# Optimization experiments

Hardware: AMD Instinct MI355X
Metric: run time of the kernel (lower is better)

The kernel has to match this reference:

```python
import jax, jax.numpy as jnp
import numpy as np
import math

B, H, S, DK = 4, 16, 2048, 64

def setup_inputs() -> dict:
    key = jax.random.key(0)
    kq, kk, kv, km = jax.random.split(key, 4)
    Q = jax.random.normal(kq, (B, H, S, DK), dtype=jnp.float32)
    K = jax.random.normal(kk, (B, H, S, DK), dtype=jnp.float32)
    V = jax.random.normal(kv, (B, H, S, DK), dtype=jnp.float32)
    # boolean mask [B, Sq, Sk]; True positions are masked out (set to -1e9)
    mask = jax.random.randint(km, (B, S, S), 0, 2).astype(jnp.bool_)
    return {"Q": Q, "K": K, "V": V, "mask": mask}

def reference(Q, K, V, mask):
    d_k = Q.shape[-1]
    # [B,H,Sq,Sk] scores
    scores = jnp.einsum('bhqd,bhkd->bhqk', Q, K) / math.sqrt(d_k)
    # mask [B,Sq,Sk] broadcasts over head dim (torch code repeats over heads)
    scores = jnp.where(mask[:, None, :, :], jnp.float32(-1e9), scores)
    attn = jax.nn.softmax(scores, axis=-1)
    out = jnp.einsum('bhqk,bhkd->bhqd', attn, V)
    return (out, attn)
```

## Files before the change

kernel.cpp:

```cpp
#include <hip/hip_runtime.h>
#include <cstdint>
#include <cstddef>

#define S_LEN 2048
#define DKD   64
#define BQ    64
#define BK    128
#define NKT   16
#define BDIM  256

typedef float f32x4 __attribute__((ext_vector_type(4)));
typedef short s16x8 __attribute__((ext_vector_type(8)));
typedef short s16x4 __attribute__((ext_vector_type(4)));
typedef unsigned int u32x4 __attribute__((ext_vector_type(4)));
typedef unsigned short u16t;
typedef unsigned long long u64t;

#define KS_OFF    0
#define KT_BYTES  (BK * DKD * 2)
#define VT_OFF    16384
#define VT_BYTES  (DKD * BK * 2)
#define PS_OFF    32768
#define PS_STRIDE 280
#define SMEM_SZ   (PS_OFF + BQ * PS_STRIDE)

__device__ __forceinline__ u16t f2bf(float f) {
  unsigned u = __builtin_bit_cast(unsigned, f);
  return (u16t)((u + 0x7FFFu + ((u >> 16) & 1u)) >> 16);
}
__device__ __forceinline__ float bf_lo(unsigned u) {
  return __builtin_bit_cast(float, u << 16);
}
__device__ __forceinline__ float bf_hi(unsigned u) {
  return __builtin_bit_cast(float, u & 0xFFFF0000u);
}

__device__ __forceinline__ void gl_lds16(const void* g, void* l) {
  typedef __attribute__((address_space(1))) void gvoid;
  typedef __attribute__((address_space(3))) void lvoid;
  __builtin_amdgcn_global_load_lds((gvoid*)(void*)g, (lvoid*)l, 16, 0, 0);
}

#define BAR_VM(N) do { asm volatile("s_waitcnt vmcnt(" #N ")\n\ts_barrier" ::: "memory"); \
                       __builtin_amdgcn_sched_barrier(0); } while (0)
#define BAR_LG()  do { asm volatile("s_waitcnt lgkmcnt(0)\n\ts_barrier" ::: "memory"); \
                       __builtin_amdgcn_sched_barrier(0); } while (0)
#define BAR_VM8() do { asm volatile("s_waitcnt vmcnt(8) lgkmcnt(0)\n\ts_barrier" ::: "memory"); \
                       __builtin_amdgcn_sched_barrier(0); } while (0)

__global__ __launch_bounds__(256)
void prologue(const unsigned char* __restrict__ Mg, const float* __restrict__ Kg,
              const float* __restrict__ Vg, u64t* __restrict__ bits,
              u16t* __restrict__ Kws, u16t* __restrict__ Vws) {
  __shared__ float scr[BK][DKD + 1];
  __shared__ int mflag_s;
  const int tid = threadIdx.x;
  const int bid = blockIdx.x;

  if (bid < 1024) {
    int f = 0;
    for (int i = tid; i < 4096; i += 256) if ((i & 3) && Mg[i]) f = 1;
    if (tid == 0) mflag_s = 0;
    __syncthreads();
    if (f) mflag_s = 1;
    __syncthreads();
    const int mstride = mflag_s ? 1 : 4;

    const int row = bid * 8 + (tid >> 5);
    const int wd  = tid & 31;
    const size_t kbase = (size_t)row * S_LEN + (size_t)wd * 64;
    u64t word = 0;
    if (mstride == 1) {
      const u64t* p = (const u64t*)(Mg + kbase);
      #pragma unroll
      for (int i = 0; i < 8; ++i) {
        u64t x = p[i];
        u64t nz = x | (x >> 4); nz |= nz >> 2; nz |= nz >> 1;
        nz &= 0x0101010101010101ull;
        word |= ((nz * 0x0102040810204080ull) >> 56) << (8 * i);
      }
    } else {
      const unsigned* p = (const unsigned*)Mg + kbase;
      #pragma unroll
      for (int i = 0; i < 64; ++i) word |= (u64t)(p[i] ? 1u : 0u) << i;
    }
    bits[(size_t)row * 32 + wd] = word;
  } else if (bid < 2048) {
    const int kb = bid - 1024;
    const float* src = Kg + (size_t)kb * (BK * DKD);
    u16t* dst = Kws + (size_t)kb * (BK * DKD);
    #pragma unroll
    for (int i = 0; i < 4; ++i) {
      int c = tid + 256 * i;
      int row = c >> 3, y = c & 7;
      int oc = y ^ (row & 7);
      const float4* s4 = (const float4*)(src + row * DKD + 8 * oc);
      float4 a = s4[0], b = s4[1];
      s16x8 h = { (short)f2bf(a.x), (short)f2bf(a.y), (short)f2bf(a.z), (short)f2bf(a.w),
                  (short)f2bf(b.x), (short)f2bf(b.y), (short)f2bf(b.z), (short)f2bf(b.w) };
      *(s16x8*)(dst + row * DKD + 8 * y) = h;
    }
  } else {
    const int vb = bid - 2048;
    const float4* src = (const float4*)(Vg + (size_t)vb * (BK * DKD));
    #pragma unroll
    for (int i = 0; i < 8; ++i) {
      int c = tid + 256 * i;
      float4 v = src[c];
      int k = c >> 4, d0 = (c & 15) * 4;
      scr[k][d0] = v.x; scr[k][d0 + 1] = v.y; scr[k][d0 + 2] = v.z; scr[k][d0 + 3] = v.w;
    }
    __syncthreads();
    u16t* dst = Vws + (size_t)vb * (DKD * BK);
    #pragma unroll
    for (int i = 0; i < 8; ++i) {
      int c = tid + 256 * i;
      int dv = c >> 5, y = c & 31;
      int k0 = 4 * (y ^ (dv & 7));
      ushort4 h = make_ushort4(f2bf(scr[k0][dv]), f2bf(scr[k0 + 1][dv]),
                               f2bf(scr[k0 + 2][dv]), f2bf(scr[k0 + 3][dv]));
      *(ushort4*)(dst + dv * BK + 4 * y) = h;
    }
  }
}

__global__ __launch_bounds__(256)
void attn_ws(const float* __restrict__ Qg, const u16t* __restrict__ Kws,
             const u16t* __restrict__ Vws, const u64t* __restrict__ bits,
             float* __restrict__ outg, float* __restrict__ attng) {
  __shared__ char smem[SMEM_SZ];
  const int tid = threadIdx.x;
  const int p = blockIdx.x;
  const int qb = (p >> 3) & 31;
  const int bh = (p & 7) + 8 * (p >> 8);
  const int b  = bh >> 4;
  const int lane = tid & 63, wv = tid >> 6;
  const int cl = lane & 15, g = lane >> 4;
  const int qrow = qb * BQ + 16 * wv + cl;
  const int swzK = (cl & 7) << 4;
  const int swzV = (cl & 7) << 3;

  const char* Kbh = (const char*)Kws + (size_t)bh * NKT * KT_BYTES;
  const char* Vbh = (const char*)Vws + (size_t)bh * NKT * VT_BYTES;
  const u64t* bitR = bits + (size_t)(b * S_LEN + qrow) * 32;
  float* attnQ = attng + ((size_t)bh * S_LEN + (size_t)qb * BQ) * S_LEN;

  float* oRow[4];
  #pragma unroll
  for (int r = 0; r < 4; ++r)
    oRow[r] = outg + (size_t)(bh * S_LEN + qb * BQ + 16 * wv + 4 * g + r) * DKD + cl;

  s16x8 aq0, aq1;
  {
    const float* qr = Qg + ((size_t)bh * S_LEN + qrow) * DKD;
    float x[8], y[8];
    *(float4*)(x)     = *(const float4*)(qr + 8 * g);
    *(float4*)(x + 4) = *(const float4*)(qr + 8 * g + 4);
    *(float4*)(y)     = *(const float4*)(qr + 32 + 8 * g);
    *(float4*)(y + 4) = *(const float4*)(qr + 32 + 8 * g + 4);
    #pragma unroll
    for (int j = 0; j < 8; ++j) { aq0[j] = (short)f2bf(x[j]); aq1[j] = (short)f2bf(y[j]); }
  }

  auto stageK = [&](int kt, int off) {
    const char* src = Kbh + (size_t)kt * KT_BYTES + wv * 4096 + lane * 16;
    #pragma unroll
    for (int t = 0; t < 4; ++t)
      gl_lds16(src + t * 1024, (void*)(smem + off + wv * 4096 + t * 1024));
  };
  auto stageV = [&](int kt) {
    const char* src = Vbh + (size_t)kt * VT_BYTES + wv * 4096 + lane * 16;
    #pragma unroll
    for (int t = 0; t < 4; ++t)
      gl_lds16(src + t * 1024, (void*)(smem + VT_OFF + wv * 4096 + t * 1024));
  };

  float lsum = 0.f;
  stageK(0, KS_OFF);
  for (int kt = 0; kt < NKT; ++kt) {
    const int cur = (kt & 1) ? VT_OFF : KS_OFF;
    if (kt + 1 < NKT) {
      stageK(kt + 1, (kt & 1) ? KS_OFF : VT_OFF);
      BAR_VM(4);
    } else {
      BAR_VM(0);
    }
    ulonglong2 bw = *(const ulonglong2*)(bitR + 2 * kt);
    #pragma unroll
    for (int s = 0; s < 8; ++s) {
      const char* rb = smem + cur + (16 * s + cl) * 128;
      s16x8 k0 = *(const s16x8*)(rb + ((16 * g) ^ swzK));
      s16x8 k1 = *(const s16x8*)(rb + ((64 + 16 * g) ^ swzK));
      f32x4 acc = {0.f, 0.f, 0.f, 0.f};
      acc = __builtin_amdgcn_mfma_f32_16x16x32_bf16(k0, aq0, acc, 0, 0, 0);
      acc = __builtin_amdgcn_mfma_f32_16x16x32_bf16(k1, aq1, acc, 0, 0, 0);
      unsigned nib = (unsigned)(((s < 4) ? bw.x : bw.y) >> (16 * (s & 3) + 4 * g)) & 0xFu;
      #pragma unroll
      for (int r = 0; r < 4; ++r)
        lsum += ((nib >> r) & 1) ? 0.f : __expf(acc[r] * 0.125f);
    }
    BAR_LG();
  }
  lsum += __shfl_xor(lsum, 16);
  lsum += __shfl_xor(lsum, 32);
  const float rinv = 1.f / lsum;

  f32x4 accpv[4];
  #pragma unroll
  for (int db = 0; db < 4; ++db) accpv[db] = (f32x4){0.f, 0.f, 0.f, 0.f};

  stageK(0, KS_OFF);
  stageV(0);
  BAR_VM(0);
  for (int kt = 0; kt < NKT; ++kt) {
    ulonglong2 bw = *(const ulonglong2*)(bitR + 2 * kt);
    char* pbase = smem + PS_OFF + (16 * wv + cl) * PS_STRIDE;

    #pragma unroll
    for (int ks = 0; ks < 4; ++ks) {
      f32x4 qa[2];
      #pragma unroll
      for (int sp = 0; sp < 2; ++sp) {
        int s = 2 * ks + sp;
        const char* rb = smem + KS_OFF + (16 * s + cl) * 128;
        s16x8 k0 = *(const s16x8*)(rb + ((16 * g) ^ swzK));
        s16x8 k1 = *(const s16x8*)(rb + ((64 + 16 * g) ^ swzK));
        f32x4 acc = {0.f, 0.f, 0.f, 0.f};
        acc = __builtin_amdgcn_mfma_f32_16x16x32_bf16(k0, aq0, acc, 0, 0, 0);
        acc = __builtin_amdgcn_mfma_f32_16x16x32_bf16(k1, aq1, acc, 0, 0, 0);
        qa[sp] = acc;
      }
      unsigned hw[4];
      #pragma unroll
      for (int sp = 0; sp < 2; ++sp) {
        int s = 2 * ks + sp;
        unsigned nib = (unsigned)(((s < 4) ? bw.x : bw.y) >> (16 * (s & 3) + 4 * g)) & 0xFu;
        #pragma unroll
        for (int rr = 0; rr < 2; ++rr) {
          float p0 = ((nib >> (2 * rr)) & 1)     ? 0.f : __expf(qa[sp][2 * rr] * 0.125f) * rinv;
          float p1 = ((nib >> (2 * rr + 1)) & 1) ? 0.f : __expf(qa[sp][2 * rr + 1] * 0.125f) * rinv;
          hw[2 * sp + rr] = (unsigned)f2bf(p0) | ((unsigned)f2bf(p1) << 16);
        }
      }
      *(uint2*)(pbase + 64 * ks + 8 * g)      = make_uint2(hw[0], hw[1]);
      *(uint2*)(pbase + 64 * ks + 32 + 8 * g) = make_uint2(hw[2], hw[3]);
      s16x8 pa = __builtin_bit_cast(s16x8, (u32x4){hw[0], hw[1], hw[2], hw[3]});
      #pragma unroll
      for (int db = 0; db < 4; ++db) {
        const char* vrow = smem + VT_OFF + (16 * db + cl) * 256;
        s16x4 v0 = *(const s16x4*)(vrow + ((64 * ks + 8 * g) ^ swzV));
        s16x4 v1 = *(const s16x4*)(vrow + ((64 * ks + 32 + 8 * g) ^ swzV));
        s16x8 vb = __builtin_shufflevector(v0, v1, 0, 1, 2, 3, 4, 5, 6, 7);
        accpv[db] = __builtin_amdgcn_mfma_f32_16x16x32_bf16(pa, vb, accpv[db], 0, 0, 0);
      }
    }

    BAR_LG();

    if (kt + 1 < NKT) { stageK(kt + 1, KS_OFF); stageV(kt + 1); }

    #pragma unroll
    for (int i = 0; i < 4; ++i) {
      int c = tid + 256 * i;
      int q = c >> 4, ch = c & 15;
      u32x4 d = *(const u32x4*)(smem + PS_OFF + q * PS_STRIDE + ch * 16);
      f32x4 lo = { bf_lo(d.x), bf_hi(d.x), bf_lo(d.y), bf_hi(d.y) };
      f32x4 hi = { bf_lo(d.z), bf_hi(d.z), bf_lo(d.w), bf_hi(d.w) };
      float* dst = attnQ + (size_t)q * S_LEN + kt * BK + ch * 8;
      __builtin_nontemporal_store(lo, (f32x4*)dst);
      __builtin_nontemporal_store(hi, (f32x4*)(dst + 4));
    }

    if (kt + 1 < NKT) BAR_VM8();
  }

  #pragma unroll
  for (int db = 0; db < 4; ++db)
    #pragma unroll
    for (int r = 0; r < 4; ++r)
      oRow[r][16 * db] = accpv[db][r];
}

#define FB_KSTR 144
#define FB_VOFF (BK * FB_KSTR)
#define FB_VSTR 272
#define FB_POFF (FB_VOFF + DKD * FB_VSTR)
#define FB_SMEM (FB_POFF + BQ * FB_VSTR)

__global__ __launch_bounds__(256)
void attn_fb(const float* __restrict__ Qg, const float* __restrict__ Kg,
             const float* __restrict__ Vg, const unsigned char* __restrict__ Mg,
             float* __restrict__ outg, float* __restrict__ attng) {
  __shared__ char smem[FB_SMEM];
  __shared__ int mflag_s;
  const int tid = threadIdx.x;
  const int p = blockIdx.x;
  const int qb = (p >> 3) & 31;
  const int bh = (p & 7) + 8 * (p >> 8);
  const int b  = bh >> 4;

  int f = 0;
  for (int i = tid; i < 4096; i += BDIM) if ((i & 3) && Mg[i]) f = 1;
  if (tid == 0) mflag_s = 0;
  __syncthreads();
  if (f) mflag_s = 1;
  __syncthreads();
  const int mstride = mflag_s ? 1 : 4;

  const int lane = tid & 63, wv = tid >> 6;
  const int cl = lane & 15, g = lane >> 4;
  const int q0 = qb * BQ + 16 * wv + 4 * g;

  const float* Kbh = Kg + (size_t)bh * S_LEN * DKD;
  const float* Vbh = Vg + (size_t)bh * S_LEN * DKD;

  float* aRow[4]; float* oRow[4]; const unsigned char* mRow[4];
  #pragma unroll
  for (int r = 0; r < 4; ++r) {
    aRow[r] = attng + (size_t)(bh * S_LEN + q0 + r) * S_LEN + cl;
    oRow[r] = outg + (size_t)(bh * S_LEN + q0 + r) * DKD + cl;
    mRow[r] = Mg + ((size_t)(b * S_LEN + q0 + r) * S_LEN + cl) * (size_t)mstride;
  }

  s16x8 aq0, aq1;
  {
    const float* qrow = Qg + ((size_t)bh * S_LEN + qb * BQ + 16 * wv + cl) * DKD;
    float x[8], y[8];
    *(float4*)(x)     = *(const float4*)(qrow + 8 * g);
    *(float4*)(x + 4) = *(const float4*)(qrow + 8 * g + 4);
    *(float4*)(y)     = *(const float4*)(qrow + 32 + 8 * g);
    *(float4*)(y + 4) = *(const float4*)(qrow + 32 + 8 * g + 4);
    #pragma unroll
    for (int j = 0; j < 8; ++j) { aq0[j] = (short)f2bf(x[j]); aq1[j] = (short)f2bf(y[j]); }
  }

  float lsum[4] = {0.f, 0.f, 0.f, 0.f};
  for (int kt = 0; kt < NKT; ++kt) {
    const float4* ksrc = (const float4*)(Kbh + (size_t)kt * (BK * DKD));
    #pragma unroll
    for (int it = 0; it < 8; ++it) {
      int c = tid + BDIM * it;
      float4 v = ksrc[c];
      *(ushort4*)(smem + (c >> 4) * FB_KSTR + (c & 15) * 8) =
          make_ushort4(f2bf(v.x), f2bf(v.y), f2bf(v.z), f2bf(v.w));
    }
    __syncthreads();
    #pragma unroll
    for (int s = 0; s < 8; ++s) {
      s16x8 b0 = *(const s16x8*)(smem + (16 * s + cl) * FB_KSTR + 16 * g);
      s16x8 b1 = *(const s16x8*)(smem + (16 * s + cl) * FB_KSTR + 64 + 16 * g);
      f32x4 acc = {0.f, 0.f, 0.f, 0.f};
      acc = __builtin_amdgcn_mfma_f32_16x16x32_bf16(aq0, b0, acc, 0, 0, 0);
      acc = __builtin_amdgcn_mfma_f32_16x16x32_bf16(aq1, b1, acc, 0, 0, 0);
      #pragma unroll
      for (int r = 0; r < 4; ++r) {
        bool mk = mRow[r][(size_t)(kt * BK + 16 * s) * mstride] != 0;
        lsum[r] += mk ? 0.f : __expf(acc[r] * 0.125f);
      }
    }
    __syncthreads();
  }
  float rinv[4];
  #pragma unroll
  for (int r = 0; r < 4; ++r) {
    float l = lsum[r];
    #pragma unroll
    for (int d = 1; d < 16; d <<= 1) l += __shfl_xor(l, d);
    rinv[r] = 1.f / l;
  }

  f32x4 accpv[4];
  #pragma unroll
  for (int db = 0; db < 4; ++db) accpv[db] = (f32x4){0.f, 0.f, 0.f, 0.f};

  for (int kt = 0; kt < NKT; ++kt) {
    const float4* ksrc = (const float4*)(Kbh + (size_t)kt * (BK * DKD));
    #pragma unroll
    for (int it = 0; it < 8; ++it) {
      int c = tid + BDIM * it;
      float4 v = ksrc[c];
      *(ushort4*)(smem + (c >> 4) * FB_KSTR + (c & 15) * 8) =
          make_ushort4(f2bf(v.x), f2bf(v.y), f2bf(v.z), f2bf(v.w));
    }
    const float4* vsrc = (const float4*)(Vbh + (size_t)kt * (BK * DKD));
    #pragma unroll
    for (int it = 0; it < 8; ++it) {
      int c = tid + BDIM * it;
      float4 v = vsrc[c];
      int k = c >> 4, d0 = (c & 15) * 4;
      *(u16t*)(smem + FB_VOFF + (d0 + 0) * FB_VSTR + k * 2) = f2bf(v.x);
      *(u16t*)(smem + FB_VOFF + (d0 + 1) * FB_VSTR + k * 2) = f2bf(v.y);
      *(u16t*)(smem + FB_VOFF + (d0 + 2) * FB_VSTR + k * 2) = f2bf(v.z);
      *(u16t*)(smem + FB_VOFF + (d0 + 3) * FB_VSTR + k * 2) = f2bf(v.w);
    }
    __syncthreads();

    #pragma unroll
    for (int ks = 0; ks < 4; ++ks) {
      f32x4 qa[2];
      #pragma unroll
      for (int sp = 0; sp < 2; ++sp) {
        int s = 2 * ks + sp;
        s16x8 b0 = *(const s16x8*)(smem + (16 * s + cl) * FB_KSTR + 16 * g);
        s16x8 b1 = *(const s16x8*)(smem + (16 * s + cl) * FB_KSTR + 64 + 16 * g);
        f32x4 acc = {0.f, 0.f, 0.f, 0.f};
        acc = __builtin_amdgcn_mfma_f32_16x16x32_bf16(aq0, b0, acc, 0, 0, 0);
        acc = __builtin_amdgcn_mfma_f32_16x16x32_bf16(aq1, b1, acc, 0, 0, 0);
        qa[sp] = acc;
      }
      #pragma unroll
      for (int sp = 0; sp < 2; ++sp) {
        int s = 2 * ks + sp;
        #pragma unroll
        for (int r = 0; r < 4; ++r) {
          bool mk = mRow[r][(size_t)(kt * BK + 16 * s) * mstride] != 0;
          float pv = mk ? 0.f : __expf(qa[sp][r] * 0.125f) * rinv[r];
          __builtin_nontemporal_store(pv, aRow[r] + kt * BK + 16 * s);
          *(u16t*)(smem + FB_POFF + (16 * wv + 4 * g + r) * FB_VSTR +
                   (32 * ks + 16 * sp + cl) * 2) = f2bf(pv);
        }
      }
      s16x4 p0 = *(const s16x4*)(smem + FB_POFF + (16 * wv + cl) * FB_VSTR + (32 * ks + 4 * g) * 2);
      s16x4 p1 = *(const s16x4*)(smem + FB_POFF + (16 * wv + cl) * FB_VSTR + (32 * ks + 16 + 4 * g) * 2);
      s16x8 pa = __builtin_shufflevector(p0, p1, 0, 1, 2, 3, 4, 5, 6, 7);
      #pragma unroll
      for (int db = 0; db < 4; ++db) {
        s16x4 v0 = *(const s16x4*)(smem + FB_VOFF + (16 * db + cl) * FB_VSTR + (32 * ks + 4 * g) * 2);
        s16x4 v1 = *(const s16x4*)(smem + FB_VOFF + (16 * db + cl) * FB_VSTR + (32 * ks + 16 + 4 * g) * 2);
        s16x8 vb = __builtin_shufflevector(v0, v1, 0, 1, 2, 3, 4, 5, 6, 7);
        accpv[db] = __builtin_amdgcn_mfma_f32_16x16x32_bf16(pa, vb, accpv[db], 0, 0, 0);
      }
    }
    __syncthreads();
  }

  #pragma unroll
  for (int db = 0; db < 4; ++db)
    #pragma unroll
    for (int r = 0; r < 4; ++r)
      oRow[r][16 * db] = accpv[db][r];
}

extern "C" void kernel_launch(void* const* d_in, const int* in_sizes, int n_in,
                              void* d_out, int out_size, void* d_ws, size_t ws_size,
                              hipStream_t stream) {
  const float* Q = (const float*)d_in[0];
  const float* K = (const float*)d_in[1];
  const float* V = (const float*)d_in[2];
  const unsigned char* M = (const unsigned char*)d_in[3];
  float* out = (float*)d_out;
  float* attn = out + (size_t)4 * 16 * S_LEN * DKD;

  const size_t BITS_SZ = (size_t)4 * S_LEN * 32 * 8;
  const size_t KWS_SZ  = (size_t)64 * NKT * BK * DKD * 2;
  const size_t VWS_SZ  = (size_t)64 * NKT * DKD * BK * 2;
  if (ws_size >= BITS_SZ + KWS_SZ + VWS_SZ) {
    u64t* bits = (u64t*)d_ws;
    u16t* Kws = (u16t*)((char*)d_ws + BITS_SZ);
    u16t* Vws = (u16t*)((char*)d_ws + BITS_SZ + KWS_SZ);
    prologue<<<3072, 256, 0, stream>>>(M, K, V, bits, Kws, Vws);
    attn_ws<<<2048, BDIM, 0, stream>>>(Q, Kws, Vws, bits, out, attn);
  } else {
    attn_fb<<<2048, BDIM, 0, stream>>>(Q, K, V, M, out, attn);
  }
}
```

Before: 348.5 us.

## Process four query strips per block, fusing next strip's row-sum pass into current PV pass

Each block now handles four consecutive 64-row query strips instead of one, and the grid shrinks to 512 blocks. The row-sum (first) pass for strip st is folded into the second pass of strip st-1, so K tiles are loaded from LDS once and used for both, removing a separate K sweep per strip. The goal is to cut redundant K staging and barriers. In exchange it adds extra MFMA and exp work inside the main loop and leaves fewer blocks to fill the GPU's CUs.

After: 362.8 us. 4.1% more time.

```diff
diff --git a/kernel.cpp b/kernel.cpp
--- a/kernel.cpp
+++ b/kernel.cpp
@@ -8,6 +8,7 @@
 #define BK    128
 #define NKT   16
 #define BDIM  256
+#define NSTRIP 4
 
 typedef float f32x4 __attribute__((ext_vector_type(4)));
 typedef short s16x8 __attribute__((ext_vector_type(8)));
@@ -47,6 +48,21 @@
                        __builtin_amdgcn_sched_barrier(0); } while (0)
 #define BAR_VM8() do { asm volatile("s_waitcnt vmcnt(8) lgkmcnt(0)\n\ts_barrier" ::: "memory"); \
                        __builtin_amdgcn_sched_barrier(0); } while (0)
+
+__device__ __forceinline__ void stage_k(const char* Kbh, int kt, char* smem, int off,
+                                        int wv, int lane) {
+  const char* src = Kbh + (size_t)kt * KT_BYTES + wv * 4096 + lane * 16;
+  #pragma unroll
+  for (int t = 0; t < 4; ++t)
+    gl_lds16(src + t * 1024, (void*)(smem + off + wv * 4096 + t * 1024));
+}
+__device__ __forceinline__ void stage_v(const char* Vbh, int kt, char* smem,
+                                        int wv, int lane) {
+  const char* src = Vbh + (size_t)kt * VT_BYTES + wv * 4096 + lane * 16;
+  #pragma unroll
+  for (int t = 0; t < 4; ++t)
+    gl_lds16(src + t * 1024, (void*)(smem + VT_OFF + wv * 4096 + t * 1024));
+}
 
 __global__ __launch_bounds__(256)
 void prologue(const unsigned char* __restrict__ Mg, const float* __restrict__ Kg,
@@ -124,6 +140,92 @@
   }
 }
 
+template <bool PH1>
+__device__ __forceinline__ void run_round(
+    char* smem, const char* Kbh, const char* Vbh,
+    const u64t* bitA, const u64t* bitB,
+    s16x8 aqA0, s16x8 aqA1, s16x8 aqB0, s16x8 aqB1,
+    float rinvA, float& lsumB, f32x4 (&accpv)[4],
+    float* attnA, int tid, int wv, int lane, int cl, int g, int swzK, int swzV)
+{
+  for (int kt = 0; kt < NKT; ++kt) {
+    ulonglong2 bwA = *(const ulonglong2*)(bitA + 2 * kt);
+    ulonglong2 bwB;
+    if (PH1) bwB = *(const ulonglong2*)(bitB + 2 * kt);
+    char* pbase = smem + PS_OFF + (16 * wv + cl) * PS_STRIDE;
+
+    #pragma unroll
+    for (int ks = 0; ks < 4; ++ks) {
+      f32x4 qa[2];
+      #pragma unroll
+      for (int sp = 0; sp < 2; ++sp) {
+        int s = 2 * ks + sp;
+        const char* rb = smem + KS_OFF + (16 * s + cl) * 128;
+        s16x8 k0 = *(const s16x8*)(rb + ((16 * g) ^ swzK));
+        s16x8 k1 = *(const s16x8*)(rb + ((64 + 16 * g) ^ swzK));
+        f32x4 a = {0.f, 0.f, 0.f, 0.f};
+        a = __builtin_amdgcn_mfma_f32_16x16x32_bf16(k0, aqA0, a, 0, 0, 0);
+        a = __builtin_amdgcn_mfma_f32_16x16x32_bf16(k1, aqA1, a, 0, 0, 0);
+        qa[sp] = a;
+        if (PH1) {
+          f32x4 bb = {0.f, 0.f, 0.f, 0.f};
+          bb = __builtin_amdgcn_mfma_f32_16x16x32_bf16(k0, aqB0, bb, 0, 0, 0);
+          bb = __builtin_amdgcn_mfma_f32_16x16x32_bf16(k1, aqB1, bb, 0, 0, 0);
+          unsigned nib = (unsigned)(((s < 4) ? bwB.x : bwB.y) >> (16 * (s & 3) + 4 * g)) & 0xFu;
+          #pragma unroll
+          for (int r = 0; r < 4; ++r)
+            lsumB += ((nib >> r) & 1) ? 0.f : __expf(bb[r] * 0.125f);
+        }
+      }
+      unsigned hw[4];
+      #pragma unroll
+      for (int sp = 0; sp < 2; ++sp) {
+        int s = 2 * ks + sp;
+        unsigned nib = (unsigned)(((s < 4) ? bwA.x : bwA.y) >> (16 * (s & 3) + 4 * g)) & 0xFu;
+        #pragma unroll
+        for (int rr = 0; rr < 2; ++rr) {
+          float p0 = ((nib >> (2 * rr)) & 1)     ? 0.f : __expf(qa[sp][2 * rr] * 0.125f) * rinvA;
+          float p1 = ((nib >> (2 * rr + 1)) & 1) ? 0.f : __expf(qa[sp][2 * rr + 1] * 0.125f) * rinvA;
+          hw[2 * sp + rr] = (unsigned)f2bf(p0) | ((unsigned)f2bf(p1) << 16);
+        }
+      }
+      *(uint2*)(pbase + 64 * ks + 8 * g)      = make_uint2(hw[0], hw[1]);
+      *(uint2*)(pbase + 64 * ks + 32 + 8 * g) = make_uint2(hw[2], hw[3]);
+      s16x8 pa = __builtin_bit_cast(s16x8, (u32x4){hw[0], hw[1], hw[2], hw[3]});
+      #pragma unroll
+      for (int db = 0; db < 4; ++db) {
+        const char* vrow = smem + VT_OFF + (16 * db + cl) * 256;
+        s16x4 v0 = *(const s16x4*)(vrow + ((64 * ks + 8 * g) ^ swzV));
+        s16x4 v1 = *(const s16x4*)(vrow + ((64 * ks + 32 + 8 * g) ^ swzV));
+        s16x8 vb = __builtin_shufflevector(v0, v1, 0, 1, 2, 3, 4, 5, 6, 7);
+        accpv[db] = __builtin_amdgcn_mfma_f32_16x16x32_bf16(pa, vb, accpv[db], 0, 0, 0);
+      }
+    }
+
+    BAR_LG();
+
+    if (PH1 || kt + 1 < NKT) {
+      int nk = (kt + 1) & (NKT - 1);
+      stage_k(Kbh, nk, smem, KS_OFF, wv, lane);
+      stage_v(Vbh, nk, smem, wv, lane);
+    }
+
+    #pragma unroll
+    for (int i = 0; i < 4; ++i) {
+      int c = tid + 256 * i;
+      int q = c >> 4, ch = c & 15;
+      u32x4 d = *(const u32x4*)(smem + PS_OFF + q * PS_STRIDE + ch * 16);
+      f32x4 lo = { bf_lo(d.x), bf_hi(d.x), bf_lo(d.y), bf_hi(d.y) };
+      f32x4 hi = { bf_lo(d.z), bf_hi(d.z), bf_lo(d.w), bf_hi(d.w) };
+      float* dst = attnA + (size_t)q * S_LEN + kt * BK + ch * 8;
+      __builtin_nontemporal_store(lo, (f32x4*)dst);
+      __builtin_nontemporal_store(hi, (f32x4*)(dst + 4));
+    }
+
+    BAR_VM8();
+  }
+}
+
 __global__ __launch_bounds__(256)
 void attn_ws(const float* __restrict__ Qg, const u16t* __restrict__ Kws,
              const u16t* __restrict__ Vws, const u64t* __restrict__ bits,
@@ -131,27 +233,19 @@
   __shared__ char smem[SMEM_SZ];
   const int tid = threadIdx.x;
   const int p = blockIdx.x;
-  const int qb = (p >> 3) & 31;
-  const int bh = (p & 7) + 8 * (p >> 8);
-  const int b  = bh >> 4;
+  const int sub = (p >> 3) & 7;
+  const int bh  = (p & 7) + 8 * (p >> 6);
+  const int b   = bh >> 4;
   const int lane = tid & 63, wv = tid >> 6;
   const int cl = lane & 15, g = lane >> 4;
-  const int qrow = qb * BQ + 16 * wv + cl;
   const int swzK = (cl & 7) << 4;
   const int swzV = (cl & 7) << 3;
 
   const char* Kbh = (const char*)Kws + (size_t)bh * NKT * KT_BYTES;
   const char* Vbh = (const char*)Vws + (size_t)bh * NKT * VT_BYTES;
-  const u64t* bitR = bits + (size_t)(b * S_LEN + qrow) * 32;
-  float* attnQ = attng + ((size_t)bh * S_LEN + (size_t)qb * BQ) * S_LEN;
-
-  float* oRow[4];
-  #pragma unroll
-  for (int r = 0; r < 4; ++r)
-    oRow[r] = outg + (size_t)(bh * S_LEN + qb * BQ + 16 * wv + 4 * g + r) * DKD + cl;
-
-  s16x8 aq0, aq1;
-  {
+
+  auto loadQ = [&](int st, s16x8& a0, s16x8& a1) {
+    int qrow = (sub * NSTRIP + st) * BQ + 16 * wv + cl;
     const float* qr = Qg + ((size_t)bh * S_LEN + qrow) * DKD;
     float x[8], y[8];
     *(float4*)(x)     = *(const float4*)(qr + 8 * g);
@@ -159,41 +253,48 @@
     *(float4*)(y)     = *(const float4*)(qr + 32 + 8 * g);
     *(float4*)(y + 4) = *(const float4*)(qr + 32 + 8 * g + 4);
     #pragma unroll
-    for (int j = 0; j < 8; ++j) { aq0[j] = (short)f2bf(x[j]); aq1[j] = (short)f2bf(y[j]); }
-  }
-
-  auto stageK = [&](int kt, int off) {
-    const char* src = Kbh + (size_t)kt * KT_BYTES + wv * 4096 + lane * 16;
-    #pragma unroll
-    for (int t = 0; t < 4; ++t)
-      gl_lds16(src + t * 1024, (void*)(smem + off + wv * 4096 + t * 1024));
+    for (int j = 0; j < 8; ++j) { a0[j] = (short)f2bf(x[j]); a1[j] = (short)f2bf(y[j]); }
   };
-  auto stageV = [&](int kt) {
-    const char* src = Vbh + (size_t)kt * VT_BYTES + wv * 4096 + lane * 16;
-    #pragma unroll
-    for (int t = 0; t < 4; ++t)
-      gl_lds16(src + t * 1024, (void*)(smem + VT_OFF + wv * 4096 + t * 1024));
+  auto bitPtr = [&](int st) {
+    int qrow = (sub * NSTRIP + st) * BQ + 16 * wv + cl;
+    return bits + (size_t)(b * S_LEN + qrow) * 32;
   };
+  auto attnPtr = [&](int st) {
+    return attng + ((size_t)bh * S_LEN + (size_t)(sub * NSTRIP + st) * BQ) * S_LEN;
+  };
+  auto writeOut = [&](int st, f32x4 (&acc)[4]) {
+    int q0 = (sub * NSTRIP + st) * BQ + 16 * wv + 4 * g;
+    #pragma unroll
+    for (int r = 0; r < 4; ++r) {
+      float* orow = outg + (size_t)(bh * S_LEN + q0 + r) * DKD + cl;
+      #pragma unroll
+      for (int db = 0; db < 4; ++db) orow[16 * db] = acc[db][r];
+    }
+  };
+
+  s16x8 aqA0, aqA1, aqB0, aqB1;
+  loadQ(0, aqA0, aqA1);
+  const u64t* bitA = bitPtr(0);
 
   float lsum = 0.f;
-  stageK(0, KS_OFF);
+  stage_k(Kbh, 0, smem, KS_OFF, wv, lane);
   for (int kt = 0; kt < NKT; ++kt) {
     const int cur = (kt & 1) ? VT_OFF : KS_OFF;
     if (kt + 1 < NKT) {
-      stageK(kt + 1, (kt & 1) ? KS_OFF : VT_OFF);
+      stage_k(Kbh, kt + 1, smem, (kt & 1) ? KS_OFF : VT_OFF, wv, lane);
       BAR_VM(4);
     } else {
       BAR_VM(0);
     }
-    ulonglong2 bw = *(const ulonglong2*)(bitR + 2 * kt);
+    ulonglong2 bw = *(const ulonglong2*)(bitA + 2 * kt);
     #pragma unroll
     for (int s = 0; s < 8; ++s) {
       const char* rb = smem + cur + (16 * s + cl) * 128;
       s16x8 k0 = *(const s16x8*)(rb + ((16 * g) ^ swzK));
       s16x8 k1 = *(const s16x8*)(rb + ((64 + 16 * g) ^ swzK));
       f32x4 acc = {0.f, 0.f, 0.f, 0.f};
-      acc = __builtin_amdgcn_mfma_f32_16x16x32_bf16(k0, aq0, acc, 0, 0, 0);
-      acc = __builtin_amdgcn_mfma_f32_16x16x32_bf16(k1, aq1, acc, 0, 0, 0);
+      acc = __builtin_amdgcn_mfma_f32_16x16x32_bf16(k0, aqA0, acc, 0, 0, 0);
+      acc = __builtin_amdgcn_mfma_f32_16x16x32_bf16(k1, aqA1, acc, 0, 0, 0);
       unsigned nib = (unsigned)(((s < 4) ? bw.x : bw.y) >> (16 * (s & 3) + 4 * g)) & 0xFu;
       #pragma unroll
       for (int r = 0; r < 4; ++r)
@@ -201,84 +302,42 @@
     }
     BAR_LG();
   }
+  stage_k(Kbh, 0, smem, KS_OFF, wv, lane);
+  stage_v(Vbh, 0, smem, wv, lane);
   lsum += __shfl_xor(lsum, 16);
   lsum += __shfl_xor(lsum, 32);
-  const float rinv = 1.f / lsum;
-
-  f32x4 accpv[4];
-  #pragma unroll
-  for (int db = 0; db < 4; ++db) accpv[db] = (f32x4){0.f, 0.f, 0.f, 0.f};
-
-  stageK(0, KS_OFF);
-  stageV(0);
+  float rinv = 1.f / lsum;
   BAR_VM(0);
-  for (int kt = 0; kt < NKT; ++kt) {
-    ulonglong2 bw = *(const ulonglong2*)(bitR + 2 * kt);
-    char* pbase = smem + PS_OFF + (16 * wv + cl) * PS_STRIDE;
-
-    #pragma unroll
-    for (int ks = 0; ks < 4; ++ks) {
-      f32x4 qa[2];
-      #pragma unroll
-      for (int sp = 0; sp < 2; ++sp) {
-        int s = 2 * ks + sp;
-        const char* rb = smem + KS_OFF + (16 * s + cl) * 128;
-        s16x8 k0 = *(const s16x8*)(rb + ((16 * g) ^ swzK));
-        s16x8 k1 = *(const s16x8*)(rb + ((64 + 16 * g) ^ swzK));
-        f32x4 acc = {0.f, 0.f, 0.f, 0.f};
-        acc = __builtin_amdgcn_mfma_f32_16x16x32_bf16(k0, aq0, acc, 0, 0, 0);
-        acc = __builtin_amdgcn_mfma_f32_16x16x32_bf16(k1, aq1, acc, 0, 0, 0);
-        qa[sp] = acc;
-      }
-      unsigned hw[4];
-      #pragma unroll
-      for (int sp = 0; sp < 2; ++sp) {
-        int s = 2 * ks + sp;
-        unsigned nib = (unsigned)(((s < 4) ? bw.x : bw.y) >> (16 * (s & 3) + 4 * g)) & 0xFu;
-        #pragma unroll
-        for (int rr = 0; rr < 2; ++rr) {
-          float p0 = ((nib >> (2 * rr)) & 1)     ? 0.f : __expf(qa[sp][2 * rr] * 0.125f) * rinv;
-          float p1 = ((nib >> (2 * rr + 1)) & 1) ? 0.f : __expf(qa[sp][2 * rr + 1] * 0.125f) * rinv;
-          hw[2 * sp + rr] = (unsigned)f2bf(p0) | ((unsigned)f2bf(p1) << 16);
-        }
-      }
-      *(uint2*)(pbase + 64 * ks + 8 * g)      = make_uint2(hw[0], hw[1]);
-      *(uint2*)(pbase + 64 * ks + 32 + 8 * g) = make_uint2(hw[2], hw[3]);
-      s16x8 pa = __builtin_bit_cast(s16x8, (u32x4){hw[0], hw[1], hw[2], hw[3]});
-      #pragma unroll
-      for (int db = 0; db < 4; ++db) {
-        const char* vrow = smem + VT_OFF + (16 * db + cl) * 256;
-        s16x4 v0 = *(const s16x4*)(vrow + ((64 * ks + 8 * g) ^ swzV));
-        s16x4 v1 = *(const s16x4*)(vrow + ((64 * ks + 32 + 8 * g) ^ swzV));
-        s16x8 vb = __builtin_shufflevector(v0, v1, 0, 1, 2, 3, 4, 5, 6, 7);
-        accpv[db] = __builtin_amdgcn_mfma_f32_16x16x32_bf16(pa, vb, accpv[db], 0, 0, 0);
-      }
-    }
-
-    BAR_LG();
-
-    if (kt + 1 < NKT) { stageK(kt + 1, KS_OFF); stageV(kt + 1); }
-
-    #pragma unroll
-    for (int i = 0; i < 4; ++i) {
-      int c = tid + 256 * i;
-      int q = c >> 4, ch = c & 15;
-      u32x4 d = *(const u32x4*)(smem + PS_OFF + q * PS_STRIDE + ch * 16);
-      f32x4 lo = { bf_lo(d.x), bf_hi(d.x), bf_lo(d.y), bf_hi(d.y) };
-      f32x4 hi = { bf_lo(d.z), bf_hi(d.z), bf_lo(d.w), bf_hi(d.w) };
-      float* dst = attnQ + (size_t)q * S_LEN + kt * BK + ch * 8;
-      __builtin_nontemporal_store(lo, (f32x4*)dst);
-      __builtin_nontemporal_store(hi, (f32x4*)(dst + 4));
-    }
-
-    if (kt + 1 < NKT) BAR_VM8();
-  }
-
-  #pragma unroll
-  for (int db = 0; db < 4; ++db)
-    #pragma unroll
-    for (int r = 0; r < 4; ++r)
-      oRow[r][16 * db] = accpv[db][r];
+
+  for (int st = 1; st < NSTRIP; ++st) {
+    loadQ(st, aqB0, aqB1);
+    const u64t* bitB = bitPtr(st);
+    float lsumB = 0.f;
+    f32x4 accpv[4];
+    #pragma unroll
+    for (int db = 0; db < 4; ++db) accpv[db] = (f32x4){0.f, 0.f, 0.f, 0.f};
+
+    run_round<true>(smem, Kbh, Vbh, bitA, bitB, aqA0, aqA1, aqB0, aqB1,
+                    rinv, lsumB, accpv, attnPtr(st - 1),
+                    tid, wv, lane, cl, g, swzK, swzV);
+    writeOut(st - 1, accpv);
+
+    lsumB += __shfl_xor(lsumB, 16);
+    lsumB += __shfl_xor(lsumB, 32);
+    rinv = 1.f / lsumB;
+    aqA0 = aqB0; aqA1 = aqB1; bitA = bitB;
+  }
+
+  {
+    float dummy = 0.f;
+    f32x4 accpv[4];
+    #pragma unroll
+    for (int db = 0; db < 4; ++db) accpv[db] = (f32x4){0.f, 0.f, 0.f, 0.f};
+    run_round<false>(smem, Kbh, Vbh, bitA, bitA, aqA0, aqA1, aqA0, aqA1,
+                     rinv, dummy, accpv, attnPtr(NSTRIP - 1),
+                     tid, wv, lane, cl, g, swzK, swzV);
+    writeOut(NSTRIP - 1, accpv);
+  }
 }
 
 #define FB_KSTR 144
@@ -459,7 +518,7 @@
     u16t* Kws = (u16t*)((char*)d_ws + BITS_SZ);
     u16t* Vws = (u16t*)((char*)d_ws + BITS_SZ + KWS_SZ);
     prologue<<<3072, 256, 0, stream>>>(M, K, V, bits, Kws, Vws);
-    attn_ws<<<2048, BDIM, 0, stream>>>(Q, Kws, Vws, bits, out, attn);
+    attn_ws<<<512, BDIM, 0, stream>>>(Q, Kws, Vws, bits, out, attn);
   } else {
     attn_fb<<<2048, BDIM, 0, stream>>>(Q, K, V, M, out, attn);
   }
```

## Drop LDS staging in attention kernel; read bf16 K/V directly from global

Applied to the files above, without the earlier changes.

Removes all shared-memory staging, barriers and swizzles from the main attention kernel. K and V are now read straight from global memory (bf16, V transposed to a [bh][d][S] layout) through the cache. The attention-probability tile is written directly from registers as fp32 nontemporal stores instead of being round-tripped through LDS. Launch bounds request 3 blocks per CU to raise occupancy. In exchange it gives up explicit K/V reuse and prefetch, and the direct stores write 16-byte chunks per lane that are less contiguous than before.

Result: slower. 1.002 ms (+187.5%).

```diff
diff --git a/kernel.cpp b/kernel.cpp
--- a/kernel.cpp
+++ b/kernel.cpp
@@ -16,37 +16,10 @@
 typedef unsigned short u16t;
 typedef unsigned long long u64t;
 
-#define KS_OFF    0
-#define KT_BYTES  (BK * DKD * 2)
-#define VT_OFF    16384
-#define VT_BYTES  (DKD * BK * 2)
-#define PS_OFF    32768
-#define PS_STRIDE 280
-#define SMEM_SZ   (PS_OFF + BQ * PS_STRIDE)
-
 __device__ __forceinline__ u16t f2bf(float f) {
   unsigned u = __builtin_bit_cast(unsigned, f);
   return (u16t)((u + 0x7FFFu + ((u >> 16) & 1u)) >> 16);
 }
-__device__ __forceinline__ float bf_lo(unsigned u) {
-  return __builtin_bit_cast(float, u << 16);
-}
-__device__ __forceinline__ float bf_hi(unsigned u) {
-  return __builtin_bit_cast(float, u & 0xFFFF0000u);
-}
-
-__device__ __forceinline__ void gl_lds16(const void* g, void* l) {
-  typedef __attribute__((address_space(1))) void gvoid;
-  typedef __attribute__((address_space(3))) void lvoid;
-  __builtin_amdgcn_global_load_lds((gvoid*)(void*)g, (lvoid*)l, 16, 0, 0);
-}
-
-#define BAR_VM(N) do { asm volatile("s_waitcnt vmcnt(" #N ")\n\ts_barrier" ::: "memory"); \
-                       __builtin_amdgcn_sched_barrier(0); } while (0)
-#define BAR_LG()  do { asm volatile("s_waitcnt lgkmcnt(0)\n\ts_barrier" ::: "memory"); \
-                       __builtin_amdgcn_sched_barrier(0); } while (0)
-#define BAR_VM8() do { asm volatile("s_waitcnt vmcnt(8) lgkmcnt(0)\n\ts_barrier" ::: "memory"); \
-                       __builtin_amdgcn_sched_barrier(0); } while (0)
 
 __global__ __launch_bounds__(256)
 void prologue(const unsigned char* __restrict__ Mg, const float* __restrict__ Kg,
@@ -87,21 +60,18 @@
     bits[(size_t)row * 32 + wd] = word;
   } else if (bid < 2048) {
     const int kb = bid - 1024;
-    const float* src = Kg + (size_t)kb * (BK * DKD);
-    u16t* dst = Kws + (size_t)kb * (BK * DKD);
     #pragma unroll
     for (int i = 0; i < 4; ++i) {
-      int c = tid + 256 * i;
-      int row = c >> 3, y = c & 7;
-      int oc = y ^ (row & 7);
-      const float4* s4 = (const float4*)(src + row * DKD + 8 * oc);
+      size_t cidx = (size_t)kb * 1024 + i * 256 + tid;
+      const float4* s4 = (const float4*)Kg + 2 * cidx;
       float4 a = s4[0], b = s4[1];
       s16x8 h = { (short)f2bf(a.x), (short)f2bf(a.y), (short)f2bf(a.z), (short)f2bf(a.w),
                   (short)f2bf(b.x), (short)f2bf(b.y), (short)f2bf(b.z), (short)f2bf(b.w) };
-      *(s16x8*)(dst + row * DKD + 8 * y) = h;
+      *((s16x8*)Kws + cidx) = h;
     }
   } else {
     const int vb = bid - 2048;
+    const int bh = vb >> 4, kb = vb & 15;
     const float4* src = (const float4*)(Vg + (size_t)vb * (BK * DKD));
     #pragma unroll
     for (int i = 0; i < 8; ++i) {
@@ -111,24 +81,21 @@
       scr[k][d0] = v.x; scr[k][d0 + 1] = v.y; scr[k][d0 + 2] = v.z; scr[k][d0 + 3] = v.w;
     }
     __syncthreads();
-    u16t* dst = Vws + (size_t)vb * (DKD * BK);
     #pragma unroll
     for (int i = 0; i < 8; ++i) {
       int c = tid + 256 * i;
-      int dv = c >> 5, y = c & 31;
-      int k0 = 4 * (y ^ (dv & 7));
+      int dv = c >> 5, k0 = (c & 31) * 4;
       ushort4 h = make_ushort4(f2bf(scr[k0][dv]), f2bf(scr[k0 + 1][dv]),
                                f2bf(scr[k0 + 2][dv]), f2bf(scr[k0 + 3][dv]));
-      *(ushort4*)(dst + dv * BK + 4 * y) = h;
-    }
-  }
-}
-
-__global__ __launch_bounds__(256)
-void attn_ws(const float* __restrict__ Qg, const u16t* __restrict__ Kws,
-             const u16t* __restrict__ Vws, const u64t* __restrict__ bits,
+      *(ushort4*)(Vws + ((size_t)bh * DKD + dv) * S_LEN + (size_t)kb * BK + k0) = h;
+    }
+  }
+}
+
+__global__ __launch_bounds__(256, 3)
+void attn_ws(const float* __restrict__ Qg, const u16t* __restrict__ Kbf,
+             const u16t* __restrict__ Vt, const u64t* __restrict__ bits,
              float* __restrict__ outg, float* __restrict__ attng) {
-  __shared__ char smem[SMEM_SZ];
   const int tid = threadIdx.x;
   const int p = blockIdx.x;
   const int qb = (p >> 3) & 31;
@@ -137,18 +104,11 @@
   const int lane = tid & 63, wv = tid >> 6;
   const int cl = lane & 15, g = lane >> 4;
   const int qrow = qb * BQ + 16 * wv + cl;
-  const int swzK = (cl & 7) << 4;
-  const int swzV = (cl & 7) << 3;
-
-  const char* Kbh = (const char*)Kws + (size_t)bh * NKT * KT_BYTES;
-  const char* Vbh = (const char*)Vws + (size_t)bh * NKT * VT_BYTES;
+
+  const u16t* Kb = Kbf + (size_t)bh * S_LEN * DKD;
+  const u16t* Vb = Vt  + (size_t)bh * DKD * S_LEN;
   const u64t* bitR = bits + (size_t)(b * S_LEN + qrow) * 32;
-  float* attnQ = attng + ((size_t)bh * S_LEN + (size_t)qb * BQ) * S_LEN;
-
-  float* oRow[4];
-  #pragma unroll
-  for (int r = 0; r < 4; ++r)
-    oRow[r] = outg + (size_t)(bh * S_LEN + qb * BQ + 16 * wv + 4 * g + r) * DKD + cl;
+  float* aRow = attng + ((size_t)bh * S_LEN + qrow) * S_LEN;
 
   s16x8 aq0, aq1;
   {
@@ -162,35 +122,15 @@
     for (int j = 0; j < 8; ++j) { aq0[j] = (short)f2bf(x[j]); aq1[j] = (short)f2bf(y[j]); }
   }
 
-  auto stageK = [&](int kt, int off) {
-    const char* src = Kbh + (size_t)kt * KT_BYTES + wv * 4096 + lane * 16;
-    #pragma unroll
-    for (int t = 0; t < 4; ++t)
-      gl_lds16(src + t * 1024, (void*)(smem + off + wv * 4096 + t * 1024));
-  };
-  auto stageV = [&](int kt) {
-    const char* src = Vbh + (size_t)kt * VT_BYTES + wv * 4096 + lane * 16;
-    #pragma unroll
-    for (int t = 0; t < 4; ++t)
-      gl_lds16(src + t * 1024, (void*)(smem + VT_OFF + wv * 4096 + t * 1024));
-  };
-
   float lsum = 0.f;
-  stageK(0, KS_OFF);
   for (int kt = 0; kt < NKT; ++kt) {
-    const int cur = (kt & 1) ? VT_OFF : KS_OFF;
-    if (kt + 1 < NKT) {
-      stageK(kt + 1, (kt & 1) ? KS_OFF : VT_OFF);
-      BAR_VM(4);
-    } else {
-      BAR_VM(0);
-    }
     ulonglong2 bw = *(const ulonglong2*)(bitR + 2 * kt);
+    const u16t* Kt = Kb + (size_t)kt * (BK * DKD);
     #pragma unroll
     for (int s = 0; s < 8; ++s) {
-      const char* rb = smem + cur + (16 * s + cl) * 128;
-      s16x8 k0 = *(const s16x8*)(rb + ((16 * g) ^ swzK));
-      s16x8 k1 = *(const s16x8*)(rb + ((64 + 16 * g) ^ swzK));
+      const u16t* kr = Kt + (16 * s + cl) * DKD;
+      s16x8 k0 = *(const s16x8*)(kr + 8 * g);
+      s16x8 k1 = *(const s16x8*)(kr + 32 + 8 * g);
       f32x4 acc = {0.f, 0.f, 0.f, 0.f};
       acc = __builtin_amdgcn_mfma_f32_16x16x32_bf16(k0, aq0, acc, 0, 0, 0);
       acc = __builtin_amdgcn_mfma_f32_16x16x32_bf16(k1, aq1, acc, 0, 0, 0);
@@ -199,7 +139,6 @@
       for (int r = 0; r < 4; ++r)
         lsum += ((nib >> r) & 1) ? 0.f : __expf(acc[r] * 0.125f);
     }
-    BAR_LG();
   }
   lsum += __shfl_xor(lsum, 16);
   lsum += __shfl_xor(lsum, 32);
@@ -209,12 +148,11 @@
   #pragma unroll
   for (int db = 0; db < 4; ++db) accpv[db] = (f32x4){0.f, 0.f, 0.f, 0.f};
 
-  stageK(0, KS_OFF);
-  stageV(0);
-  BAR_VM(0);
   for (int kt = 0; kt < NKT; ++kt) {
     ulonglong2 bw = *(const ulonglong2*)(bitR + 2 * kt);
-    char* pbase = smem + PS_OFF + (16 * wv + cl) * PS_STRIDE;
+    const u16t* Kt = Kb + (size_t)kt * (BK * DKD);
+    const u16t* Vk = Vb + (size_t)kt * BK;
+    float* aKt = aRow + kt * BK;
 
     #pragma unroll
     for (int ks = 0; ks < 4; ++ks) {
@@ -222,9 +160,9 @@
       #pragma unroll
       for (int sp = 0; sp < 2; ++sp) {
         int s = 2 * ks + sp;
-        const char* rb = smem + KS_OFF + (16 * s + cl) * 128;
-        s16x8 k0 = *(const s16x8*)(rb + ((16 * g) ^ swzK));
-        s16x8 k1 = *(const s16x8*)(rb + ((64 + 16 * g) ^ swzK));
+        const u16t* kr = Kt + (16 * s + cl) * DKD;
+        s16x8 k0 = *(const s16x8*)(kr + 8 * g);
+        s16x8 k1 = *(const s16x8*)(kr + 32 + 8 * g);
         f32x4 acc = {0.f, 0.f, 0.f, 0.f};
         acc = __builtin_amdgcn_mfma_f32_16x16x32_bf16(k0, aq0, acc, 0, 0, 0);
         acc = __builtin_amdgcn_mfma_f32_16x16x32_bf16(k1, aq1, acc, 0, 0, 0);
@@ -235,50 +173,33 @@
       for (int sp = 0; sp < 2; ++sp) {
         int s = 2 * ks + sp;
         unsigned nib = (unsigned)(((s < 4) ? bw.x : bw.y) >> (16 * (s & 3) + 4 * g)) & 0xFu;
+        f32x4 pv4;
         #pragma unroll
-        for (int rr = 0; rr < 2; ++rr) {
-          float p0 = ((nib >> (2 * rr)) & 1)     ? 0.f : __expf(qa[sp][2 * rr] * 0.125f) * rinv;
-          float p1 = ((nib >> (2 * rr + 1)) & 1) ? 0.f : __expf(qa[sp][2 * rr + 1] * 0.125f) * rinv;
-          hw[2 * sp + rr] = (unsigned)f2bf(p0) | ((unsigned)f2bf(p1) << 16);
-        }
-      }
-      *(uint2*)(pbase + 64 * ks + 8 * g)      = make_uint2(hw[0], hw[1]);
-      *(uint2*)(pbase + 64 * ks + 32 + 8 * g) = make_uint2(hw[2], hw[3]);
+        for (int r = 0; r < 4; ++r)
+          pv4[r] = ((nib >> r) & 1) ? 0.f : __expf(qa[sp][r] * 0.125f) * rinv;
+        __builtin_nontemporal_store(pv4, (f32x4*)(aKt + 16 * s + 4 * g));
+        hw[2 * sp + 0] = (unsigned)f2bf(pv4[0]) | ((unsigned)f2bf(pv4[1]) << 16);
+        hw[2 * sp + 1] = (unsigned)f2bf(pv4[2]) | ((unsigned)f2bf(pv4[3]) << 16);
+      }
       s16x8 pa = __builtin_bit_cast(s16x8, (u32x4){hw[0], hw[1], hw[2], hw[3]});
       #pragma unroll
       for (int db = 0; db < 4; ++db) {
-        const char* vrow = smem + VT_OFF + (16 * db + cl) * 256;
-        s16x4 v0 = *(const s16x4*)(vrow + ((64 * ks + 8 * g) ^ swzV));
-        s16x4 v1 = *(const s16x4*)(vrow + ((64 * ks + 32 + 8 * g) ^ swzV));
+        const u16t* vr = Vk + (size_t)(16 * db + cl) * S_LEN + 32 * ks + 4 * g;
+        s16x4 v0 = *(const s16x4*)(vr);
+        s16x4 v1 = *(const s16x4*)(vr + 16);
         s16x8 vb = __builtin_shufflevector(v0, v1, 0, 1, 2, 3, 4, 5, 6, 7);
         accpv[db] = __builtin_amdgcn_mfma_f32_16x16x32_bf16(pa, vb, accpv[db], 0, 0, 0);
       }
     }
-
-    BAR_LG();
-
-    if (kt + 1 < NKT) { stageK(kt + 1, KS_OFF); stageV(kt + 1); }
-
-    #pragma unroll
-    for (int i = 0; i < 4; ++i) {
-      int c = tid + 256 * i;
-      int q = c >> 4, ch = c & 15;
-      u32x4 d = *(const u32x4*)(smem + PS_OFF + q * PS_STRIDE + ch * 16);
-      f32x4 lo = { bf_lo(d.x), bf_hi(d.x), bf_lo(d.y), bf_hi(d.y) };
-      f32x4 hi = { bf_lo(d.z), bf_hi(d.z), bf_lo(d.w), bf_hi(d.w) };
-      float* dst = attnQ + (size_t)q * S_LEN + kt * BK + ch * 8;
-      __builtin_nontemporal_store(lo, (f32x4*)dst);
-      __builtin_nontemporal_store(hi, (f32x4*)(dst + 4));
-    }
-
-    if (kt + 1 < NKT) BAR_VM8();
-  }
-
-  #pragma unroll
-  for (int db = 0; db < 4; ++db)
-    #pragma unroll
-    for (int r = 0; r < 4; ++r)
-      oRow[r][16 * db] = accpv[db][r];
+  }
+
+  const int q0 = qb * BQ + 16 * wv + 4 * g;
+  #pragma unroll
+  for (int r = 0; r < 4; ++r) {
+    float* orow = outg + (size_t)(bh * S_LEN + q0 + r) * DKD + cl;
+    #pragma unroll
+    for (int db = 0; db < 4; ++db) orow[16 * db] = accpv[db][r];
+  }
 }
 
 #define FB_KSTR 144
@@ -452,8 +373,8 @@
   float* attn = out + (size_t)4 * 16 * S_LEN * DKD;
 
   const size_t BITS_SZ = (size_t)4 * S_LEN * 32 * 8;
-  const size_t KWS_SZ  = (size_t)64 * NKT * BK * DKD * 2;
-  const size_t VWS_SZ  = (size_t)64 * NKT * DKD * BK * 2;
+  const size_t KWS_SZ  = (size_t)64 * S_LEN * DKD * 2;
+  const size_t VWS_SZ  = (size_t)64 * DKD * S_LEN * 2;
   if (ws_size >= BITS_SZ + KWS_SZ + VWS_SZ) {
     u64t* bits = (u64t*)d_ws;
     u16t* Kws = (u16t*)((char*)d_ws + BITS_SZ);
```
